# Kernel optimization log

Hardware: AMD Instinct MI355X
Metric: run time of the kernel (lower is better)

## Reference

```python
import jax, jax.numpy as jnp
import numpy as np

B = 8192
NUM_NODES = 100000
EMB = 128
W1D, W2D, W3D = 64, 128, 256   # witness_dims
CODE = 128
HID = 64                        # hardcoded hidden_dim in WitnessExtractor / decoder
TOTW = W1D + W2D + W3D          # 448


def _linear_params(key, fan_in, fan_out):
    k1, k2 = jax.random.split(key)
    bound = 1.0 / np.sqrt(fan_in)
    w = jax.random.uniform(k1, (fan_out, fan_in), jnp.float32, -bound, bound)
    b = jax.random.uniform(k2, (fan_out,), jnp.float32, -bound, bound)
    return w, b


def setup_inputs() -> dict:
    key = jax.random.key(0)
    ks = jax.random.split(key, 12)
    u = jax.random.randint(ks[0], (B,), 0, NUM_NODES, dtype=jnp.int64 if jax.config.jax_enable_x64 else jnp.int32)
    v = jax.random.randint(ks[1], (B,), 0, NUM_NODES, dtype=u.dtype)
    emb = jax.random.normal(ks[2], (NUM_NODES, EMB), jnp.float32)
    e1_w1, e1_b1 = _linear_params(ks[3], 2 * EMB, HID)
    e1_w2, e1_b2 = _linear_params(ks[4], HID, W1D)
    e2_w1, e2_b1 = _linear_params(ks[5], 2 * EMB + W1D, HID)
    e2_w2, e2_b2 = _linear_params(ks[6], HID, W2D)
    e3_w1, e3_b1 = _linear_params(ks[7], 2 * EMB + W2D, HID)
    e3_w2, e3_b2 = _linear_params(ks[8], HID, W3D)
    trop_w = jax.random.normal(ks[9], (CODE, TOTW), jnp.float32)  # init_scale=1.0
    dec_w1, dec_b1 = _linear_params(ks[10], CODE, HID)
    dec_w2, dec_b2 = _linear_params(ks[11], HID, 1)
    return dict(u=u, v=v, emb=emb,
                e1_w1=e1_w1, e1_b1=e1_b1, e1_w2=e1_w2, e1_b2=e1_b2,
                e2_w1=e2_w1, e2_b1=e2_b1, e2_w2=e2_w2, e2_b2=e2_b2,
                e3_w1=e3_w1, e3_b1=e3_b1, e3_w2=e3_w2, e3_b2=e3_b2,
                trop_w=trop_w, dec_w1=dec_w1, dec_b1=dec_b1,
                dec_w2=dec_w2, dec_b2=dec_b2)


def _witness(x, w1, b1, w2, b2):
    h = jax.nn.relu(x @ w1.T + b1)
    return jax.nn.sigmoid(h @ w2.T + b2)


def reference(u, v, emb,
              e1_w1, e1_b1, e1_w2, e1_b2,
              e2_w1, e2_b1, e2_w2, e2_b2,
              e3_w1, e3_b1, e3_w2, e3_b2,
              trop_w, dec_w1, dec_b1, dec_w2, dec_b2):
    u_emb = emb[u]                               # [B, EMB]
    v_emb = emb[v]
    base = jnp.concatenate([u_emb, v_emb], axis=1)  # [B, 2*EMB]
    w1 = _witness(base, e1_w1, e1_b1, e1_w2, e1_b2)
    w2 = _witness(jnp.concatenate([base, w1], axis=1), e2_w1, e2_b1, e2_w2, e2_b2)
    w3 = _witness(jnp.concatenate([base, w2], axis=1), e3_w1, e3_b1, e3_w2, e3_b2)
    wit = jnp.concatenate([w1, w2, w3], axis=1)  # [B, TOTW]
    # tropical (min-plus) matmul: code[b,o] = min_j (wit[b,j] + trop_w[o,j])
    code = jnp.min(wit[:, None, :] + trop_w[None, :, :], axis=2)  # [B, CODE]
    h = jax.nn.relu(code @ dec_w1.T + dec_b1)
    return h @ dec_w2.T + dec_b2                 # [B, 1]
```

## Files before the change

kernel.cpp:

```cpp
#include <hip/hip_runtime.h>
#include <hip/hip_fp16.h>
#include <math.h>

#define BATCH 8192
#define EMB 128
#define TILE 16
#define NTHREADS 1024
#define NWAVES 16
#define CH 136
#define WITS 450
#define ENT_CAP 4096

#define OFF_E1W1 0
#define OFF_E1W2 16384
#define OFF_E2W1 20480
#define OFF_E2W2 40960
#define OFF_E3W1 49152
#define OFF_E3W2 73728
#define OFF_DW1  90112
#define OFF_DW2  98304
#define W_DENSE  98368

typedef __attribute__((ext_vector_type(8))) _Float16 v8h;
typedef __attribute__((ext_vector_type(4))) float v4f;

struct Smem {
    _Float16 XB[32 * CH];
    _Float16 W12C[24 * CH];
    _Float16 H[8 * CH];
    _Float16 CODE[16 * CH];
    _Float16 WITrm[TILE * WITS];
    unsigned int ent[ENT_CAP];
    unsigned int off[132];
};

__global__ __launch_bounds__(1024) void prep_kernel(
    const float* __restrict__ s0, const float* __restrict__ s1,
    const float* __restrict__ s2, const float* __restrict__ s3,
    const float* __restrict__ s4, const float* __restrict__ s5,
    const float* __restrict__ s6, const float* __restrict__ s7,
    const float* __restrict__ trop, _Float16* __restrict__ ws)
{
    const int b = blockIdx.x;
    const int tid = threadIdx.x;
    if (b < 25) {
        const int idx4 = (b * 1024 + tid) * 4;
        if (idx4 >= W_DENSE) return;
        const float* src; int off;
        if      (idx4 < OFF_E1W2) { src = s0; off = OFF_E1W1; }
        else if (idx4 < OFF_E2W1) { src = s1; off = OFF_E1W2; }
        else if (idx4 < OFF_E2W2) { src = s2; off = OFF_E2W1; }
        else if (idx4 < OFF_E3W1) { src = s3; off = OFF_E2W2; }
        else if (idx4 < OFF_E3W2) { src = s4; off = OFF_E3W1; }
        else if (idx4 < OFF_DW1)  { src = s5; off = OFF_E3W2; }
        else if (idx4 < OFF_DW2)  { src = s6; off = OFF_DW1;  }
        else                      { src = s7; off = OFF_DW2;  }
        const float4 v = *(const float4*)(src + (idx4 - off));
        _Float16* dst = ws + idx4;
        dst[0] = (_Float16)v.x; dst[1] = (_Float16)v.y;
        dst[2] = (_Float16)v.z; dst[3] = (_Float16)v.w;
    } else {
        const int lane = tid & 63;
        const int wave = tid >> 6;
        const int o = (b - 25) * 16 + wave;
        if (o >= 128) return;
        unsigned int* base = (unsigned int*)(ws + W_DENSE);
        unsigned int* counter = base + 131;

        const float* row = trop + (size_t)o * 448;
        float vals[7];
        float mn = 1e30f;
        #pragma unroll
        for (int it = 0; it < 7; ++it) {
            vals[it] = row[lane + it * 64];
            mn = fminf(mn, vals[it]);
        }
        mn = fminf(mn, __shfl_xor(mn, 1, 64));
        mn = fminf(mn, __shfl_xor(mn, 2, 64));
        mn = fminf(mn, __shfl_xor(mn, 4, 64));
        mn = fminf(mn, __shfl_xor(mn, 8, 64));
        mn = fminf(mn, __shfl_xor(mn, 16, 64));
        mn = fminf(mn, __shfl_xor(mn, 32, 64));
        const float thr = mn + 1.02f;

        unsigned long long masks[7];
        unsigned int n = 0;
        #pragma unroll
        for (int it = 0; it < 7; ++it) {
            masks[it] = __ballot(vals[it] <= thr);
            n += (unsigned)__popcll(masks[it]);
        }
        unsigned int beg = 0;
        if (lane == 0) beg = atomicAdd(counter, n);
        beg = (unsigned)__shfl((int)beg, 0, 64);
        if (lane == 0) base[o] = (n << 16) | (beg & 0xffffu);

        unsigned int done = beg;
        const unsigned long long ltmask = (1ull << lane) - 1ull;
        #pragma unroll
        for (int it = 0; it < 7; ++it) {
            const unsigned long long m = masks[it];
            if (vals[it] <= thr) {
                const unsigned int pos = done + (unsigned)__popcll(m & ltmask);
                if (pos < ENT_CAP) {
                    const unsigned short hb =
                        __builtin_bit_cast(unsigned short, (_Float16)vals[it]);
                    base[132 + pos] = ((unsigned)(lane + it * 64) << 16) | hb;
                }
            }
            done += (unsigned)__popcll(m);
        }
    }
}

template <int K, int STEPS0, int O, int ACT, bool CHUNKW, bool RMW>
__device__ __forceinline__ void dense_mfma(
    const _Float16* __restrict__ Wg, const float* __restrict__ bias,
    const _Float16* A0, const _Float16* A1,
    _Float16* OutC, _Float16* OutRM, int rmbase, int wave, int lane)
{
    constexpr int STEPS = K / 32;
    constexpr int NJOBS = O / 16;
    const int l15 = lane & 15;
    const int quad = lane >> 4;

    for (int nt = wave; nt < NJOBS; nt += NWAVES) {
        v4f c = {0.f, 0.f, 0.f, 0.f};
        const _Float16* wrow = Wg + (size_t)(nt * 16 + l15) * K + quad * 8;
        #pragma unroll
        for (int s = 0; s < STEPS; ++s) {
            const int g = s * 4 + quad;
            const _Float16* asrc = (s < STEPS0)
                ? (A0 + g * CH + l15 * 8)
                : (A1 + (g - STEPS0 * 4) * CH + l15 * 8);
            const v8h a = *(const v8h*)asrc;
            const v8h bfr = *(const v8h*)(wrow + s * 32);
            c = __builtin_amdgcn_mfma_f32_16x16x32_f16(a, bfr, c, 0, 0, 0);
        }
        const int o = nt * 16 + l15;
        const float bs = bias[o];
        #pragma unroll
        for (int i = 0; i < 4; ++i) {
            float vv = c[i] + bs;
            if (ACT == 0) vv = fmaxf(vv, 0.f);
            else          vv = 1.f / (1.f + __expf(-vv));
            const int m = quad * 4 + i;
            const _Float16 hv = (_Float16)vv;
            if (CHUNKW) OutC[(o >> 3) * CH + m * 8 + (o & 7)] = hv;
            if (RMW)    OutRM[m * WITS + rmbase + o] = hv;
        }
    }
}

__global__ __launch_bounds__(NTHREADS, 8) void tacit_fused_kernel(
    const int* __restrict__ u, const int* __restrict__ v,
    const float* __restrict__ emb,
    const float* __restrict__ e1_b1, const float* __restrict__ e1_b2,
    const float* __restrict__ e2_b1, const float* __restrict__ e2_b2,
    const float* __restrict__ e3_b1, const float* __restrict__ e3_b2,
    const float* __restrict__ dec_b1, const float* __restrict__ dec_b2,
    const _Float16* __restrict__ ws,
    float* __restrict__ out)
{
    __shared__ Smem S;
    const int tid = threadIdx.x;
    const int lane = tid & 63;
    const int wave = tid >> 6;
    const int row0 = blockIdx.x * TILE;

    if (tid < 512) {
        const int row = tid & 15;
        const int kq = tid >> 4;
        const int node = (kq < 16) ? u[row0 + row] : v[row0 + row];
        const int col = (kq & 15) * 8;
        const float4 f0 = *(const float4*)(emb + (size_t)node * EMB + col);
        const float4 f1 = *(const float4*)(emb + (size_t)node * EMB + col + 4);
        v8h hv;
        hv[0] = (_Float16)f0.x; hv[1] = (_Float16)f0.y;
        hv[2] = (_Float16)f0.z; hv[3] = (_Float16)f0.w;
        hv[4] = (_Float16)f1.x; hv[5] = (_Float16)f1.y;
        hv[6] = (_Float16)f1.z; hv[7] = (_Float16)f1.w;
        *(v8h*)&S.XB[kq * CH + row * 8] = hv;
    }
    {
        const unsigned int* base = (const unsigned int*)(ws + W_DENSE);
        if (tid < 33) *(uint4*)&S.off[tid * 4] = *(const uint4*)(base + tid * 4);
        *(uint4*)&S.ent[tid * 4] = *(const uint4*)(base + 132 + tid * 4);
    }
    __syncthreads();

    dense_mfma<256, 8, 64, 0, true, false>(ws + OFF_E1W1, e1_b1, S.XB, nullptr,
                                           S.H, nullptr, 0, wave, lane);
    __syncthreads();
    dense_mfma<64, 2, 64, 1, true, true>(ws + OFF_E1W2, e1_b2, S.H, nullptr,
                                         S.W12C, S.WITrm, 0, wave, lane);
    __syncthreads();

    dense_mfma<320, 8, 64, 0, true, false>(ws + OFF_E2W1, e2_b1, S.XB, S.W12C,
                                           S.H, nullptr, 0, wave, lane);
    __syncthreads();
    dense_mfma<64, 2, 128, 1, true, true>(ws + OFF_E2W2, e2_b2, S.H, nullptr,
                                          S.W12C + 8 * CH, S.WITrm, 64, wave, lane);
    __syncthreads();

    dense_mfma<384, 8, 64, 0, true, false>(ws + OFF_E3W1, e3_b1, S.XB, S.W12C + 8 * CH,
                                           S.H, nullptr, 0, wave, lane);
    __syncthreads();
    dense_mfma<64, 2, 256, 1, false, true>(ws + OFF_E3W2, e3_b2, S.H, nullptr,
                                           nullptr, S.WITrm, 192, wave, lane);
    __syncthreads();

    {
        const int r = lane & 15;
        const int cp = lane >> 4;
        const _Float16* wrow = &S.WITrm[r * WITS];
        #pragma unroll
        for (int i = 0; i < 8; ++i) {
            const int o = (wave << 3) + i;
            const unsigned int tb = S.off[o];
            const int beg = (int)(tb & 0xffffu);
            int end = beg + (int)(tb >> 16);
            end = end < ENT_CAP ? end : ENT_CAP;
            float acc = 1e30f;
            for (int idx = beg + cp; idx < end; idx += 4) {
                const unsigned int cwv = S.ent[idx];
                const int j = (int)(cwv >> 16);
                const float tv = (float)__builtin_bit_cast(
                    _Float16, (unsigned short)(cwv & 0xffffu));
                acc = fminf(acc, (float)wrow[j] + tv);
            }
            acc = fminf(acc, __shfl_xor(acc, 16, 64));
            acc = fminf(acc, __shfl_xor(acc, 32, 64));
            if (cp == 0)
                S.CODE[(o >> 3) * CH + r * 8 + (o & 7)] = (_Float16)acc;
        }
    }
    __syncthreads();

    dense_mfma<128, 4, 64, 0, true, false>(ws + OFF_DW1, dec_b1, S.CODE, nullptr,
                                           S.H, nullptr, 0, wave, lane);
    __syncthreads();

    if (tid < TILE) {
        const int r = tid;
        float s = dec_b2[0];
        const _Float16* w2 = ws + OFF_DW2;
        #pragma unroll
        for (int c = 0; c < 8; ++c) {
            const v8h hr = *(const v8h*)(&S.H[c * CH + r * 8]);
            const v8h wr = *(const v8h*)(w2 + c * 8);
            #pragma unroll
            for (int t = 0; t < 8; ++t) s += (float)hr[t] * (float)wr[t];
        }
        out[row0 + r] = s;
    }
}

extern "C" void kernel_launch(void* const* d_in, const int* in_sizes, int n_in,
                              void* d_out, int out_size, void* d_ws, size_t ws_size,
                              hipStream_t stream) {
    const int*   u      = (const int*)d_in[0];
    const int*   v      = (const int*)d_in[1];
    const float* emb    = (const float*)d_in[2];
    const float* e1_w1  = (const float*)d_in[3];
    const float* e1_b1  = (const float*)d_in[4];
    const float* e1_w2  = (const float*)d_in[5];
    const float* e1_b2  = (const float*)d_in[6];
    const float* e2_w1  = (const float*)d_in[7];
    const float* e2_b1  = (const float*)d_in[8];
    const float* e2_w2  = (const float*)d_in[9];
    const float* e2_b2  = (const float*)d_in[10];
    const float* e3_w1  = (const float*)d_in[11];
    const float* e3_b1  = (const float*)d_in[12];
    const float* e3_w2  = (const float*)d_in[13];
    const float* e3_b2  = (const float*)d_in[14];
    const float* trop_w = (const float*)d_in[15];
    const float* dec_w1 = (const float*)d_in[16];
    const float* dec_b1 = (const float*)d_in[17];
    const float* dec_w2 = (const float*)d_in[18];
    const float* dec_b2 = (const float*)d_in[19];
    float* out = (float*)d_out;
    _Float16* ws = (_Float16*)d_ws;

    hipMemsetAsync((char*)d_ws + (size_t)W_DENSE * 2 + 131 * 4, 0, 4, stream);

    prep_kernel<<<33, 1024, 0, stream>>>(
        e1_w1, e1_w2, e2_w1, e2_w2, e3_w1, e3_w2, dec_w1, dec_w2, trop_w, ws);

    tacit_fused_kernel<<<BATCH / TILE, NTHREADS, 0, stream>>>(
        u, v, emb,
        e1_b1, e1_b2, e2_b1, e2_b2, e3_b1, e3_b2, dec_b1, dec_b2,
        ws, out);
}
```

Measured before the change: 147.6 us.

## Add ILP via dual MFMA accumulators, interleaved min-plus loops, parallel decoder tail

```diff
diff --git a/kernel.cpp b/kernel.cpp
--- a/kernel.cpp
+++ b/kernel.cpp
@@ -120,23 +120,33 @@
     _Float16* OutC, _Float16* OutRM, int rmbase, int wave, int lane)
 {
     constexpr int STEPS = K / 32;
+    static_assert(STEPS % 2 == 0, "even steps");
     constexpr int NJOBS = O / 16;
     const int l15 = lane & 15;
     const int quad = lane >> 4;
 
     for (int nt = wave; nt < NJOBS; nt += NWAVES) {
-        v4f c = {0.f, 0.f, 0.f, 0.f};
+        v4f c0 = {0.f, 0.f, 0.f, 0.f};
+        v4f c1 = {0.f, 0.f, 0.f, 0.f};
         const _Float16* wrow = Wg + (size_t)(nt * 16 + l15) * K + quad * 8;
         #pragma unroll
-        for (int s = 0; s < STEPS; ++s) {
-            const int g = s * 4 + quad;
-            const _Float16* asrc = (s < STEPS0)
-                ? (A0 + g * CH + l15 * 8)
-                : (A1 + (g - STEPS0 * 4) * CH + l15 * 8);
-            const v8h a = *(const v8h*)asrc;
-            const v8h bfr = *(const v8h*)(wrow + s * 32);
-            c = __builtin_amdgcn_mfma_f32_16x16x32_f16(a, bfr, c, 0, 0, 0);
-        }
+        for (int s = 0; s < STEPS; s += 2) {
+            const int g0 = s * 4 + quad;
+            const int g1 = (s + 1) * 4 + quad;
+            const _Float16* a0p = (s < STEPS0)
+                ? (A0 + g0 * CH + l15 * 8)
+                : (A1 + (g0 - STEPS0 * 4) * CH + l15 * 8);
+            const _Float16* a1p = ((s + 1) < STEPS0)
+                ? (A0 + g1 * CH + l15 * 8)
+                : (A1 + (g1 - STEPS0 * 4) * CH + l15 * 8);
+            const v8h a0 = *(const v8h*)a0p;
+            const v8h b0 = *(const v8h*)(wrow + s * 32);
+            const v8h a1 = *(const v8h*)a1p;
+            const v8h b1 = *(const v8h*)(wrow + (s + 1) * 32);
+            c0 = __builtin_amdgcn_mfma_f32_16x16x32_f16(a0, b0, c0, 0, 0, 0);
+            c1 = __builtin_amdgcn_mfma_f32_16x16x32_f16(a1, b1, c1, 0, 0, 0);
+        }
+        const v4f c = c0 + c1;
         const int o = nt * 16 + l15;
         const float bs = bias[o];
         #pragma unroll
@@ -168,6 +178,11 @@
     const int wave = tid >> 6;
     const int row0 = blockIdx.x * TILE;
 
+    {
+        const unsigned int* base = (const unsigned int*)(ws + W_DENSE);
+        if (tid < 33) *(uint4*)&S.off[tid * 4] = *(const uint4*)(base + tid * 4);
+        *(uint4*)&S.ent[tid * 4] = *(const uint4*)(base + 132 + tid * 4);
+    }
     if (tid < 512) {
         const int row = tid & 15;
         const int kq = tid >> 4;
@@ -182,11 +197,6 @@
         hv[6] = (_Float16)f1.z; hv[7] = (_Float16)f1.w;
         *(v8h*)&S.XB[kq * CH + row * 8] = hv;
     }
-    {
-        const unsigned int* base = (const unsigned int*)(ws + W_DENSE);
-        if (tid < 33) *(uint4*)&S.off[tid * 4] = *(const uint4*)(base + tid * 4);
-        *(uint4*)&S.ent[tid * 4] = *(const uint4*)(base + 132 + tid * 4);
-    }
     __syncthreads();
 
     dense_mfma<256, 8, 64, 0, true, false>(ws + OFF_E1W1, e1_b1, S.XB, nullptr,
@@ -214,25 +224,44 @@
         const int r = lane & 15;
         const int cp = lane >> 4;
         const _Float16* wrow = &S.WITrm[r * WITS];
+        float acc[8];
+        int idx[8], end8[8];
         #pragma unroll
         for (int i = 0; i < 8; ++i) {
             const int o = (wave << 3) + i;
             const unsigned int tb = S.off[o];
             const int beg = (int)(tb & 0xffffu);
-            int end = beg + (int)(tb >> 16);
-            end = end < ENT_CAP ? end : ENT_CAP;
-            float acc = 1e30f;
-            for (int idx = beg + cp; idx < end; idx += 4) {
-                const unsigned int cwv = S.ent[idx];
-                const int j = (int)(cwv >> 16);
-                const float tv = (float)__builtin_bit_cast(
-                    _Float16, (unsigned short)(cwv & 0xffffu));
-                acc = fminf(acc, (float)wrow[j] + tv);
+            int e = beg + (int)(tb >> 16);
+            e = e < ENT_CAP ? e : ENT_CAP;
+            idx[i] = beg + cp;
+            end8[i] = e;
+            acc[i] = 1e30f;
+        }
+        bool any = true;
+        while (any) {
+            any = false;
+            #pragma unroll
+            for (int i = 0; i < 8; ++i) {
+                if (idx[i] < end8[i]) {
+                    const unsigned int cwv = S.ent[idx[i]];
+                    const int j = (int)(cwv >> 16);
+                    const float tv = (float)__builtin_bit_cast(
+                        _Float16, (unsigned short)(cwv & 0xffffu));
+                    acc[i] = fminf(acc[i], (float)wrow[j] + tv);
+                    idx[i] += 4;
+                    any = true;
+                }
             }
-            acc = fminf(acc, __shfl_xor(acc, 16, 64));
-            acc = fminf(acc, __shfl_xor(acc, 32, 64));
-            if (cp == 0)
-                S.CODE[(o >> 3) * CH + r * 8 + (o & 7)] = (_Float16)acc;
+        }
+        #pragma unroll
+        for (int i = 0; i < 8; ++i) {
+            float a = acc[i];
+            a = fminf(a, __shfl_xor(a, 16, 64));
+            a = fminf(a, __shfl_xor(a, 32, 64));
+            if (cp == 0) {
+                const int o = (wave << 3) + i;
+                S.CODE[(o >> 3) * CH + r * 8 + (o & 7)] = (_Float16)a;
+            }
         }
     }
     __syncthreads();
@@ -241,18 +270,22 @@
                                            S.H, nullptr, 0, wave, lane);
     __syncthreads();
 
-    if (tid < TILE) {
-        const int r = tid;
-        float s = dec_b2[0];
+    if (tid < 64) {
+        const int r = lane & 15;
+        const int part = lane >> 4;
         const _Float16* w2 = ws + OFF_DW2;
-        #pragma unroll
-        for (int c = 0; c < 8; ++c) {
+        float s = 0.f;
+        #pragma unroll
+        for (int q = 0; q < 2; ++q) {
+            const int c = part + q * 4;
             const v8h hr = *(const v8h*)(&S.H[c * CH + r * 8]);
             const v8h wr = *(const v8h*)(w2 + c * 8);
             #pragma unroll
             for (int t = 0; t < 8; ++t) s += (float)hr[t] * (float)wr[t];
         }
-        out[row0 + r] = s;
+        s += __shfl_xor(s, 16, 64);
+        s += __shfl_xor(s, 32, 64);
+        if (part == 0) out[row0 + r] = s + dec_b2[0];
     }
 }
 
```

Result: no change. 145.5 us (-1.4%).
